# Kernel optimization log

Hardware: AMD Instinct MI355X
Metric: run time of the kernel (lower is better)

## Reference

```python
import jax, jax.numpy as jnp
import numpy as np

N_OR = 8          # orientations of the SE(2) discretization
BN_EPS = 1e-5


def _rotate_kernel(W, theta):
    """Rotate a spatial kernel [..., k, k] about its center by theta.
    Bilinear interpolation, zeros outside the kernel support."""
    k = W.shape[-1]
    c = (k - 1) / 2.0
    ys, xs = jnp.meshgrid(jnp.arange(k, dtype=jnp.float32) - c,
                          jnp.arange(k, dtype=jnp.float32) - c, indexing="ij")
    cos, sin = jnp.cos(theta), jnp.sin(theta)
    sy = cos * ys - sin * xs + c   # source coords: rotate sample grid by -theta
    sx = sin * ys + cos * xs + c
    y0 = jnp.floor(sy).astype(jnp.int32)
    x0 = jnp.floor(sx).astype(jnp.int32)
    wy = (sy - y0).astype(W.dtype)
    wx = (sx - x0).astype(W.dtype)

    def gather(yi, xi):
        valid = ((yi >= 0) & (yi < k) & (xi >= 0) & (xi < k)).astype(W.dtype)
        yc = jnp.clip(yi, 0, k - 1)
        xc = jnp.clip(xi, 0, k - 1)
        return W[..., yc, xc] * valid

    return (gather(y0, x0) * (1 - wy) * (1 - wx)
            + gather(y0, x0 + 1) * (1 - wy) * wx
            + gather(y0 + 1, x0) * wy * (1 - wx)
            + gather(y0 + 1, x0 + 1) * wy * wx)


def _thetas():
    return 2.0 * jnp.pi * jnp.arange(N_OR, dtype=jnp.float32) / N_OR


def _lift(x, W):
    """LiftM2Cartesian. x: [B,Cin,H,W] (pre-padded), W: [Cout,Cin,k,k].
    Returns [B,Cout,8,H',W']."""
    Wr = jax.vmap(lambda t: _rotate_kernel(W, t))(_thetas())  # [8,Cout,Cin,k,k]
    co = W.shape[0]
    Wf = Wr.reshape((N_OR * co,) + W.shape[1:])
    y = jax.lax.conv_general_dilated(x, Wf, (1, 1), "VALID",
                                     dimension_numbers=("NCHW", "OIHW", "NCHW"))
    B, _, H, Wd = y.shape
    return y.reshape(B, N_OR, co, H, Wd).transpose(0, 2, 1, 3, 4)


def _gconv(x, K):
    """ConvM2Cartesian. x: [B,Cin,8,H,W] (spatially pre-padded),
    K: [Cout,Cin,8,k,k]. Output orientation m uses the kernel spatially
    rotated by theta_m with the orientation axis cyclically shifted by m."""
    cout, cin, _, k, _ = K.shape
    # orient_idx[m, o] = (o - m) mod 8
    orient_idx = (jnp.arange(N_OR)[None, :] - jnp.arange(N_OR)[:, None]) % N_OR
    Kshift = jnp.moveaxis(K[:, :, orient_idx], 2, 0)        # [8m,Cout,Cin,8o,k,k]
    Km = jax.vmap(_rotate_kernel)(Kshift, _thetas())         # [8m,Cout,Cin,8o,k,k]
    Kf = Km.reshape(N_OR * cout, cin * N_OR, k, k)
    B, _, _, H, Wd = x.shape
    xf = x.reshape(B, cin * N_OR, H, Wd)
    y = jax.lax.conv_general_dilated(xf, Kf, (1, 1), "VALID",
                                     dimension_numbers=("NCHW", "OIHW", "NCHW"))
    Ho, Wo = y.shape[-2:]
    return y.reshape(B, N_OR, cout, Ho, Wo).transpose(0, 2, 1, 3, 4)


def _bn3d(x, gamma, beta):
    """BatchNorm3d (training-mode batch statistics). x: [B,C,O,H,W]."""
    mean = jnp.mean(x, axis=(0, 2, 3, 4), keepdims=True)
    var = jnp.mean((x - mean) ** 2, axis=(0, 2, 3, 4), keepdims=True)
    g = gamma.reshape(1, -1, 1, 1, 1)
    b = beta.reshape(1, -1, 1, 1, 1)
    return g * (x - mean) * jax.lax.rsqrt(var + BN_EPS) + b


def _pad_m2(x, p):
    return jnp.pad(x, ((0, 0), (0, 0), (0, 0), (p, p), (p, p)), mode="reflect")


def setup_inputs() -> dict:
    key = jax.random.key(0)
    ks = jax.random.split(key, 8)
    c = 16
    cin = 3
    x = jax.random.normal(ks[0], (2, cin, 256, 256), dtype=jnp.float32)
    lift_w = jax.random.normal(ks[1], (c, cin, 7, 7), dtype=jnp.float32) / np.sqrt(cin * 49)
    w1 = jax.random.normal(ks[2], (c, c, N_OR, 5, 5), dtype=jnp.float32) / np.sqrt(c * N_OR * 25)
    w2 = jax.random.normal(ks[3], (c, c, N_OR, 5, 5), dtype=jnp.float32) / np.sqrt(c * N_OR * 25)
    w3 = jax.random.normal(ks[4], (c, c, N_OR, 5, 5), dtype=jnp.float32) / np.sqrt(c * N_OR * 25)
    w4 = jax.random.normal(ks[5], (c, c, N_OR, 1, 1), dtype=jnp.float32) / np.sqrt(c * N_OR)
    final_w = jax.random.normal(ks[6], (1, c), dtype=jnp.float32) / np.sqrt(c)
    ones = jnp.ones((c,), dtype=jnp.float32)
    zeros = jnp.zeros((c,), dtype=jnp.float32)
    return {"x": x, "lift_w": lift_w, "w1": w1, "w2": w2, "w3": w3, "w4": w4,
            "final_w": final_w,
            "g0": ones, "b0": zeros, "g1": ones, "b1": zeros, "g2": ones,
            "b2": zeros, "g3": ones, "b3": zeros, "g4": ones, "b4": zeros}


def reference(x, lift_w, w1, w2, w3, w4, final_w,
              g0, b0, g1, b1, g2, b2, g3, b3, g4, b4):
    # lift: ReflectionPad2d(3) -> LiftM2Cartesian(7) -> BN3d -> ReLU
    xp = jnp.pad(x, ((0, 0), (0, 0), (3, 3), (3, 3)), mode="reflect")
    h = jax.nn.relu(_bn3d(_lift(xp, lift_w), g0, b0))          # [B,16,8,H,W]
    # conv1..3: ReflectionPadM2(2) -> ConvM2Cartesian(5) -> BN3d -> ReLU (Dropout3d is identity in eval)
    h = jax.nn.relu(_bn3d(_gconv(_pad_m2(h, 2), w1), g1, b1))
    h = jax.nn.relu(_bn3d(_gconv(_pad_m2(h, 2), w2), g2, b2))
    h = jax.nn.relu(_bn3d(_gconv(_pad_m2(h, 2), w3), g3, b3))
    # conv4: 1x1 group conv -> BN3d -> ReLU
    h = jax.nn.relu(_bn3d(_gconv(h, w4), g4, b4))
    # MaxProjectM2: max over orientation axis
    h = jnp.max(h, axis=2)                                     # [B,16,H,W]
    # final 1x1 conv (no bias) + sigmoid
    return jax.nn.sigmoid(jnp.einsum("bchw,oc->bohw", h, final_w))
```

## Files before the change

kernel.cpp:

```cpp
#include <hip/hip_runtime.h>
#include <hip/hip_bf16.h>
#include <math.h>

#define HW 65536
#define WID 256
#define NOR 8
#define PLANE_C (NOR * HW)
#define PLANE_B (16 * NOR * HW)
#define BN_N 1048576.0f
#define NHWC_STRIDE 136

typedef __attribute__((ext_vector_type(8)))  short  short8;
typedef __attribute__((ext_vector_type(4)))  short  short4v;
typedef __attribute__((ext_vector_type(16))) float  float16;
typedef __attribute__((ext_vector_type(4)))  float  float4v;

__device__ __forceinline__ float b2f(short s) {
    union { unsigned int u; float f; } c;
    c.u = ((unsigned int)(unsigned short)s) << 16;
    return c.f;
}
__device__ __forceinline__ short f2b(float f) {
    union { __hip_bfloat16 h; short s; } c;
    c.h = __float2bfloat16(f);
    return c.s;
}

__global__ void detect_k(const void* __restrict__ x, int* __restrict__ flag) {
    __shared__ int bad;
    if (threadIdx.x == 0) bad = 0;
    __syncthreads();
    const __hip_bfloat16* p = (const __hip_bfloat16*)x;
    for (int i = threadIdx.x; i < 4096; i += 256) {
        float v = __bfloat162float(p[i]);
        if (!(fabsf(v) < 1e4f)) atomicOr(&bad, 1);
    }
    __syncthreads();
    if (threadIdx.x == 0) *flag = bad ? 0 : 1;
}

#define CVT_TOTAL 551392
__global__ void cvt_all_k(const void* p0, const void* p1, const void* p2, const void* p3,
                          const void* p4, const void* p5, const void* p6, const void* p7,
                          const void* p8, const void* p9, const void* p10, const void* p11,
                          const void* p12, const void* p13, const void* p14, const void* p15,
                          const void* p16, float* __restrict__ dst, const int* __restrict__ flag) {
    int i = blockIdx.x * 512 + threadIdx.x;
    if (i >= CVT_TOTAL) return;
    const void* src; int off;
    if      (i < 393216) { src = p0;  off = 0; }
    else if (i < 395568) { src = p1;  off = 393216; }
    else if (i < 446768) { src = p2;  off = 395568; }
    else if (i < 497968) { src = p3;  off = 446768; }
    else if (i < 549168) { src = p4;  off = 497968; }
    else if (i < 551216) { src = p5;  off = 549168; }
    else if (i < 551232) { src = p6;  off = 551216; }
    else if (i < 551248) { src = p7;  off = 551232; }
    else if (i < 551264) { src = p8;  off = 551248; }
    else if (i < 551280) { src = p9;  off = 551264; }
    else if (i < 551296) { src = p10; off = 551280; }
    else if (i < 551312) { src = p11; off = 551296; }
    else if (i < 551328) { src = p12; off = 551312; }
    else if (i < 551344) { src = p13; off = 551328; }
    else if (i < 551360) { src = p14; off = 551344; }
    else if (i < 551376) { src = p15; off = 551360; }
    else                 { src = p16; off = 551376; }
    int j = i - off;
    dst[i] = (*flag) ? __bfloat162float(((const __hip_bfloat16*)src)[j])
                     : ((const float*)src)[j];
}

__device__ float rot_sample(const float* __restrict__ W, int k, float theta, int i, int j) {
    float c = 0.5f * (float)(k - 1);
    float ys = (float)i - c, xs = (float)j - c;
    float cs = cosf(theta), sn = sinf(theta);
    float sy = cs * ys - sn * xs + c;
    float sx = sn * ys + cs * xs + c;
    float fy = floorf(sy), fx = floorf(sx);
    int y0 = (int)fy, x0 = (int)fx;
    float wy = sy - fy, wx = sx - fx;
    float v00 = (y0 >= 0 && y0 < k && x0 >= 0 && x0 < k)                 ? W[y0 * k + x0]           : 0.f;
    float v01 = (y0 >= 0 && y0 < k && x0 + 1 >= 0 && x0 + 1 < k)         ? W[y0 * k + x0 + 1]       : 0.f;
    float v10 = (y0 + 1 >= 0 && y0 + 1 < k && x0 >= 0 && x0 < k)         ? W[(y0 + 1) * k + x0]     : 0.f;
    float v11 = (y0 + 1 >= 0 && y0 + 1 < k && x0 + 1 >= 0 && x0 + 1 < k) ? W[(y0 + 1) * k + x0 + 1] : 0.f;
    return v00 * (1 - wy) * (1 - wx) + v01 * (1 - wy) * wx
         + v10 * wy * (1 - wx) + v11 * wy * wx;
}

__device__ __forceinline__ float theta_of(int m) {
    return (6.2831855f * (float)m) / 8.0f;
}

__device__ __forceinline__ int mirror(int i) {
    i = i < 0 ? -i : i;
    return i >= WID ? (2 * WID - 2 - i) : i;
}

#define PK_BLIFT 20480
#define PK_BG 409600
#define PK_TOTAL (PK_BLIFT + 3 * PK_BG + 16384)
__global__ void mega_pack_k(const float* __restrict__ lwF, const float* __restrict__ w1F,
                            const float* __restrict__ w2F, const float* __restrict__ w3F,
                            const float* __restrict__ w4F,
                            __hip_bfloat16* __restrict__ Blift, __hip_bfloat16* __restrict__ Bg1,
                            __hip_bfloat16* __restrict__ Bg2, __hip_bfloat16* __restrict__ Bg3,
                            __hip_bfloat16* __restrict__ B1, float* __restrict__ statsL) {
    int idx = blockIdx.x * 256 + threadIdx.x;
    if (idx < 160) statsL[idx] = 0.f;
    if (idx >= PK_TOTAL) return;
    if (idx < PK_BLIFT) {
        int n = idx / 160, k = idx % 160;
        float v = 0.f;
        if (k < 147) {
            int c = n >> 3, o = n & 7;
            int ci = k / 49, s = k % 49;
            v = rot_sample(lwF + (c * 3 + ci) * 49, 7, theta_of(o), s / 7, s % 7);
        }
        Blift[idx] = __float2bfloat16(v);
        return;
    }
    idx -= PK_BLIFT;
    if (idx < 3 * PK_BG) {
        int l = idx / PK_BG;
        int r = idx - l * PK_BG;
        const float* w = (l == 0) ? w1F : ((l == 1) ? w2F : w3F);
        __hip_bfloat16* Bg = (l == 0) ? Bg1 : ((l == 1) ? Bg2 : Bg3);
        int j = r & 7;
        int n = (r >> 3) & 127;
        int kc4 = (r >> 10) & 3;
        int sq = r >> 12;
        int s = sq % 25, q = sq / 25;
        int ch = q * 32 + kc4 * 8 + j;
        int co = n >> 3, m = n & 7, ci = ch >> 3, o = ch & 7;
        int oo = (o - m + 8) & 7;
        Bg[r] = __float2bfloat16(
            rot_sample(w + ((co * 16 + ci) * 8 + oo) * 25, 5, theta_of(m), s / 5, s % 5));
        return;
    }
    idx -= 3 * PK_BG;
    {
        int n = idx >> 7, ch = idx & 127;
        int co = n >> 3, m = n & 7, ci = ch >> 3, o = ch & 7;
        B1[idx] = __float2bfloat16(w4F[(co * 16 + ci) * 8 + ((o - m + 8) & 7)]);
    }
}

__device__ __forceinline__ void stats_reduce8(const float16* acc, int lane, int l31,
                                              float* sred) {
#pragma unroll
    for (int nt = 0; nt < 4; nt++) {
        float sv = 0.f, s2v = 0.f;
#pragma unroll
        for (int g = 0; g < 2; g++)
#pragma unroll
            for (int r = 0; r < 16; r++) {
                float v = acc[g * 4 + nt][r];
                sv += v;
                s2v += v * v;
            }
#pragma unroll
        for (int off = 1; off <= 4; off <<= 1) {
            sv += __shfl_xor(sv, off);
            s2v += __shfl_xor(s2v, off);
        }
        sv += __shfl_xor(sv, 32);
        s2v += __shfl_xor(s2v, 32);
        if ((lane & 39) == 0) {
            int c = nt * 4 + (l31 >> 3);
            atomicAdd(&sred[c], sv);
            atomicAdd(&sred[16 + c], s2v);
        }
    }
}

__global__ __launch_bounds__(256, 2) void lift_fused_k(const float* __restrict__ xF,
                                                       const __hip_bfloat16* __restrict__ Bh,
                                                       __hip_bfloat16* __restrict__ nh_out,
                                                       float* __restrict__ stats) {
    __shared__ float Xs[3 * 484];
    __shared__ short tb[32768];
    __shared__ float sred[32];
    const short* B = (const short*)Bh;
    int tid = threadIdx.x;
    if (tid < 32) sred[tid] = 0.f;
    int tile = blockIdx.x;
    int b = blockIdx.y;
    int tx0 = (tile & 15) << 4, ty0 = (tile >> 4) << 4;
    for (int i = tid; i < 1452; i += 256) {
        int ci = i / 484, p = i - ci * 484;
        int yl = p / 22, xl = p - yl * 22;
        int gy = mirror(ty0 - 3 + yl), gx = mirror(tx0 - 3 + xl);
        Xs[i] = xF[((size_t)b * 3 + ci) * HW + gy * WID + gx];
    }
    __syncthreads();
    int wave = tid >> 6, lane = tid & 63;
    int l31 = lane & 31, half = lane >> 5;
    float16 acc[8];
#pragma unroll
    for (int i = 0; i < 8; i++) acc[i] = (float16)0.f;
    int pxl0 = wave * 64 + l31;
    int py0 = pxl0 >> 4, px0 = pxl0 & 15;
    int py1 = (pxl0 + 32) >> 4, px1 = (pxl0 + 32) & 15;
    const short* bp = B + (size_t)l31 * 160 + half * 8;
#pragma unroll
    for (int ks = 0; ks < 10; ks++) {
        short8 a0, a1;
#pragma unroll
        for (int j = 0; j < 8; j++) {
            int k = ks * 16 + half * 8 + j;
            float v0 = 0.f, v1 = 0.f;
            if (k < 147) {
                int ci = (k < 49) ? 0 : ((k < 98) ? 1 : 2);
                int s = k - ci * 49;
                int sy = s / 7, sx = s - sy * 7;
                v0 = Xs[ci * 484 + (py0 + sy) * 22 + px0 + sx];
                v1 = Xs[ci * 484 + (py1 + sy) * 22 + px1 + sx];
            }
            a0[j] = f2b(v0);
            a1[j] = f2b(v1);
        }
#pragma unroll
        for (int nt = 0; nt < 4; nt++) {
            short8 bb = *(const short8*)(bp + nt * 32 * 160 + ks * 16);
            acc[nt]     = __builtin_amdgcn_mfma_f32_32x32x16_bf16(a0, bb, acc[nt], 0, 0, 0);
            acc[4 + nt] = __builtin_amdgcn_mfma_f32_32x32x16_bf16(a1, bb, acc[4 + nt], 0, 0, 0);
        }
    }
#pragma unroll
    for (int g = 0; g < 2; g++)
#pragma unroll
        for (int nt = 0; nt < 4; nt++) {
            int ch = nt * 32 + l31;
#pragma unroll
            for (int r4 = 0; r4 < 4; r4++) {
                int pxb = wave * 64 + g * 32 + 8 * r4 + 4 * half;
#pragma unroll
                for (int i = 0; i < 4; i++)
                    tb[(pxb + i) * 128 + ch] = f2b(acc[g * 4 + nt][r4 * 4 + i]);
            }
        }
    __syncthreads();
    short* outp = (short*)nh_out + (size_t)b * HW * NHWC_STRIDE;
    for (int i = tid; i < 4096; i += 256) {
        int pxl = i >> 4, seg = i & 15;
        int y = ty0 + (pxl >> 4), x = tx0 + (pxl & 15);
        *(short8*)(outp + ((size_t)y * WID + x) * NHWC_STRIDE + seg * 8) =
            *(const short8*)&tb[pxl * 128 + seg * 8];
    }
    stats_reduce8(acc, lane, l31, sred);
    __syncthreads();
    if (tid < 16) {
        atomicAdd(&stats[tid * 2], sred[tid]);
        atomicAdd(&stats[tid * 2 + 1], sred[16 + tid]);
    }
}

__global__ __launch_bounds__(256, 3) void gconv_mfma_k(const __hip_bfloat16* __restrict__ nh_in,
                                                       const __hip_bfloat16* __restrict__ Bgh,
                                                       __hip_bfloat16* __restrict__ nh_out,
                                                       const float* __restrict__ statsPrev,
                                                       const float* __restrict__ gPrev,
                                                       const float* __restrict__ bPrev,
                                                       float* __restrict__ statsNew) {
    __shared__ short Au[16384];
    __shared__ float ssl[32];
    __shared__ float sred[32];
    const short* nhwc = (const short*)nh_in;
    const short* Bg = (const short*)Bgh;
    int bid = blockIdx.x;
    int xcd = bid & 7, q2 = bid >> 3;
    int nhalf = q2 & 1, qt = q2 >> 1;
    int b = xcd >> 2, band = xcd & 3;
    int tx0 = (qt & 15) << 4;
    int ty0 = (band << 6) + ((qt >> 4) << 4);
    int tid = threadIdx.x;
    if (tid < 32) sred[tid] = 0.f;
    if (tid < 16) {
        float mean = statsPrev[tid * 2] / BN_N;
        float var = statsPrev[tid * 2 + 1] / BN_N - mean * mean;
        float sc = gPrev[tid] * rsqrtf(var + 1e-5f);
        ssl[tid * 2] = sc;
        ssl[tid * 2 + 1] = bPrev[tid] - mean * sc;
    }
    int w = tid >> 6, lane = tid & 63;
    int l15 = lane & 15, l4 = lane >> 4;
    float4v acc[16];
#pragma unroll
    for (int i = 0; i < 16; i++) acc[i] = (float4v)0.f;
    const size_t bbase = (size_t)b * HW;
    const int nb = nhalf << 6;

    for (int q = 0; q < 4; q++) {
        __syncthreads();
        for (int i = tid; i < 1600; i += 256) {
            int kc = i / 400, p = i - kc * 400;
            int yl = p / 20, xl = p - yl * 20;
            int gy = mirror(ty0 - 2 + yl);
            int gx = mirror(tx0 - 2 + xl);
            short8 raw = *(const short8*)(nhwc + (bbase + gy * WID + gx) * NHWC_STRIDE
                                          + q * 32 + kc * 8);
            int c = q * 4 + kc;
            float sc = ssl[c * 2], sh = ssl[c * 2 + 1];
            short8 ov;
#pragma unroll
            for (int e = 0; e < 8; e++)
                ov[e] = f2b(fmaxf(fmaf(b2f(raw[e]), sc, sh), 0.f));
            *(short8*)&Au[(kc * 441 + yl * 21 + xl) * 8] = ov;
        }
        __syncthreads();
        for (int s = 0; s < 25; s++) {
            int dy = s / 5 - 2, dx = s % 5 - 2;
            int abase = l4 * 441 + ((w << 2) + 2 + dy) * 21 + (l15 + 2 + dx);
            const short* brow = Bg + ((size_t)(((q * 25 + s) << 2) + l4) * 128 + nb + l15) * 8;
            short8 a0 = *(const short8*)&Au[abase * 8];
            short8 a1 = *(const short8*)&Au[(abase + 21) * 8];
            short8 a2 = *(const short8*)&Au[(abase + 42) * 8];
            short8 a3 = *(const short8*)&Au[(abase + 63) * 8];
#pragma unroll
            for (int nt = 0; nt < 4; nt++) {
                short8 bb = *(const short8*)(brow + nt * 128);
                acc[nt]      = __builtin_amdgcn_mfma_f32_16x16x32_bf16(a0, bb, acc[nt], 0, 0, 0);
                acc[4 + nt]  = __builtin_amdgcn_mfma_f32_16x16x32_bf16(a1, bb, acc[4 + nt], 0, 0, 0);
                acc[8 + nt]  = __builtin_amdgcn_mfma_f32_16x16x32_bf16(a2, bb, acc[8 + nt], 0, 0, 0);
                acc[12 + nt] = __builtin_amdgcn_mfma_f32_16x16x32_bf16(a3, bb, acc[12 + nt], 0, 0, 0);
            }
        }
    }

    __syncthreads();
#pragma unroll
    for (int ag = 0; ag < 4; ag++) {
        int pxb = ((w << 2) + ag) * 16 + (l4 << 2);
#pragma unroll
        for (int nt = 0; nt < 4; nt++) {
            int nl = nt * 16 + l15;
#pragma unroll
            for (int r = 0; r < 4; r++)
                Au[(pxb + r) * 64 + nl] = f2b(acc[ag * 4 + nt][r]);
        }
    }
    __syncthreads();
    short* outp = (short*)nh_out;
    for (int i = tid; i < 2048; i += 256) {
        int pxl = i >> 3, seg = i & 7;
        int y = ty0 + (pxl >> 4), x = tx0 + (pxl & 15);
        *(short8*)(outp + (bbase + y * WID + x) * NHWC_STRIDE + nb + seg * 8) =
            *(const short8*)&Au[pxl * 64 + seg * 8];
    }
#pragma unroll
    for (int nt = 0; nt < 4; nt++) {
        float sv = 0.f, s2v = 0.f;
#pragma unroll
        for (int ag = 0; ag < 4; ag++)
#pragma unroll
            for (int r = 0; r < 4; r++) {
                float v = acc[ag * 4 + nt][r];
                sv += v;
                s2v += v * v;
            }
#pragma unroll
        for (int off = 1; off <= 4; off <<= 1) {
            sv += __shfl_xor(sv, off);
            s2v += __shfl_xor(s2v, off);
        }
        sv += __shfl_xor(sv, 16);
        s2v += __shfl_xor(s2v, 16);
        sv += __shfl_xor(sv, 32);
        s2v += __shfl_xor(s2v, 32);
        if ((lane & 7) == 0 && l4 == 0) {
            int c = (nhalf << 3) + (nt << 1) + (l15 >> 3);
            atomicAdd(&sred[c], sv);
            atomicAdd(&sred[16 + c], s2v);
        }
    }
    __syncthreads();
    if (tid < 16) {
        atomicAdd(&statsNew[tid * 2], sred[tid]);
        atomicAdd(&statsNew[tid * 2 + 1], sred[16 + tid]);
    }
}

__global__ __launch_bounds__(256, 2) void conv1x1_gemm_k(const __hip_bfloat16* __restrict__ nh,
                                                         const __hip_bfloat16* __restrict__ B1h,
                                                         __hip_bfloat16* __restrict__ outP,
                                                         const float* __restrict__ statsPrev,
                                                         const float* __restrict__ gPrev,
                                                         const float* __restrict__ bPrev,
                                                         float* __restrict__ statsNew) {
    __shared__ float sred[32];
    __shared__ float ssl[32];
    const short* nhwc = (const short*)nh;
    const short* B1 = (const short*)B1h;
    int tid = threadIdx.x;
    if (tid < 32) sred[tid] = 0.f;
    if (tid < 16) {
        float mean = statsPrev[tid * 2] / BN_N;
        float var = statsPrev[tid * 2 + 1] / BN_N - mean * mean;
        float sc = gPrev[tid] * rsqrtf(var + 1e-5f);
        ssl[tid * 2] = sc;
        ssl[tid * 2 + 1] = bPrev[tid] - mean * sc;
    }
    __syncthreads();
    int b = blockIdx.y;
    int wave = tid >> 6, lane = tid & 63;
    int l31 = lane & 31, half = lane >> 5;
    int p0 = blockIdx.x * 256 + wave * 64;
    float16 acc[8];
#pragma unroll
    for (int i = 0; i < 8; i++) acc[i] = (float16)0.f;
    const short* a0p = nhwc + ((size_t)b * HW + p0 + l31) * NHWC_STRIDE + half * 8;
    const short* a1p = a0p + 32 * NHWC_STRIDE;
    const short* bp  = B1 + (size_t)l31 * 128 + half * 8;
#pragma unroll
    for (int ks = 0; ks < 8; ks++) {
        short8 r0 = *(const short8*)(a0p + ks * 16);
        short8 r1 = *(const short8*)(a1p + ks * 16);
        int c = ks * 2 + half;
        float sc = ssl[c * 2], sh = ssl[c * 2 + 1];
        short8 a0, a1;
#pragma unroll
        for (int e = 0; e < 8; e++) {
            a0[e] = f2b(fmaxf(fmaf(b2f(r0[e]), sc, sh), 0.f));
            a1[e] = f2b(fmaxf(fmaf(b2f(r1[e]), sc, sh), 0.f));
        }
#pragma unroll
        for (int nt = 0; nt < 4; nt++) {
            short8 bb = *(const short8*)(bp + nt * 32 * 128 + ks * 16);
            acc[nt]     = __builtin_amdgcn_mfma_f32_32x32x16_bf16(a0, bb, acc[nt], 0, 0, 0);
            acc[4 + nt] = __builtin_amdgcn_mfma_f32_32x32x16_bf16(a1, bb, acc[4 + nt], 0, 0, 0);
        }
    }
    short* outb = (short*)outP + (size_t)b * PLANE_B;
#pragma unroll
    for (int g = 0; g < 2; g++)
#pragma unroll
        for (int nt = 0; nt < 4; nt++) {
            int n = nt * 32 + l31;
#pragma unroll
            for (int r4 = 0; r4 < 4; r4++) {
                int base = 8 * r4 + 4 * half;
                short4v v;
                v[0] = f2b(acc[g * 4 + nt][r4 * 4 + 0]);
                v[1] = f2b(acc[g * 4 + nt][r4 * 4 + 1]);
                v[2] = f2b(acc[g * 4 + nt][r4 * 4 + 2]);
                v[3] = f2b(acc[g * 4 + nt][r4 * 4 + 3]);
                *(short4v*)(outb + (size_t)n * HW + p0 + g * 32 + base) = v;
            }
        }
    stats_reduce8(acc, lane, l31, sred);
    __syncthreads();
    if (tid < 16) {
        atomicAdd(&statsNew[tid * 2], sred[tid]);
        atomicAdd(&statsNew[tid * 2 + 1], sred[16 + tid]);
    }
}

__global__ void final_k(const __hip_bfloat16* __restrict__ inP, const float* __restrict__ stats,
                        const float* __restrict__ g, const float* __restrict__ beta,
                        const float* __restrict__ fw, void* __restrict__ out,
                        const int* __restrict__ flag) {
    __shared__ float ssl[32];
    if (threadIdx.x < 16) {
        int c = threadIdx.x;
        float mean = stats[c * 2] / BN_N;
        float var = stats[c * 2 + 1] / BN_N - mean * mean;
        float sc = g[c] * rsqrtf(var + 1e-5f);
        ssl[c * 2] = sc;
        ssl[c * 2 + 1] = beta[c] - mean * sc;
    }
    __syncthreads();
    int i = blockIdx.x * blockDim.x + threadIdx.x;
    int b = i >> 16, pix = i & 65535;
    const short* inp = (const short*)inP;
    float acc = 0.f;
#pragma unroll
    for (int co = 0; co < 16; co++) {
        float sc = ssl[co * 2], sh = ssl[co * 2 + 1];
        float mx = 0.f;
        const short* p = inp + (size_t)b * PLANE_B + (size_t)co * PLANE_C + pix;
#pragma unroll
        for (int m = 0; m < 8; m++) mx = fmaxf(mx, fmaf(b2f(p[m * HW]), sc, sh));
        acc = fmaf(fw[co], mx, acc);
    }
    float r = 1.f / (1.f + expf(-acc));
    if (*flag)
        ((__hip_bfloat16*)out)[i] = __float2bfloat16(r);
    else
        ((float*)out)[i] = r;
}

extern "C" void kernel_launch(void* const* d_in, const int* in_sizes, int n_in,
                              void* d_out, int out_size, void* d_ws, size_t ws_size,
                              hipStream_t stream) {
    float* ws = (float*)d_ws;
    __hip_bfloat16* planarB = (__hip_bfloat16*)ws;
    __hip_bfloat16* nhwcA = (__hip_bfloat16*)(ws + 8388608);
    __hip_bfloat16* nhwcB = (__hip_bfloat16*)(ws + 17301504);
    __hip_bfloat16* Bg1   = (__hip_bfloat16*)(ws + 26214400);
    __hip_bfloat16* Bg2   = (__hip_bfloat16*)(ws + 26419200);
    __hip_bfloat16* Bg3   = (__hip_bfloat16*)(ws + 26624000);
    __hip_bfloat16* Blift = (__hip_bfloat16*)(ws + 26828800);
    __hip_bfloat16* B1    = (__hip_bfloat16*)(ws + 26839040);
    float* xF  = ws + 26847232;
    float* lwF = xF + 393216;
    float* w1F = lwF + 2352;
    float* w2F = w1F + 51200;
    float* w3F = w2F + 51200;
    float* w4F = w3F + 51200;
    float* fwF = w4F + 2048;
    float* gbF = fwF + 16;
    float* statsL = ws + 27398624;
    int*   flag   = (int*)(statsL + 160);

    detect_k<<<1, 256, 0, stream>>>(d_in[0], flag);
    cvt_all_k<<<(CVT_TOTAL + 511) / 512, 512, 0, stream>>>(
        d_in[0], d_in[1], d_in[2], d_in[3], d_in[4], d_in[5], d_in[6], d_in[7], d_in[8],
        d_in[9], d_in[10], d_in[11], d_in[12], d_in[13], d_in[14], d_in[15], d_in[16],
        xF, flag);

    mega_pack_k<<<(PK_TOTAL + 255) / 256, 256, 0, stream>>>(
        lwF, w1F, w2F, w3F, w4F, Blift, Bg1, Bg2, Bg3, B1, statsL);

    lift_fused_k<<<dim3(256, 2), 256, 0, stream>>>(xF, Blift, nhwcA, statsL);

    __hip_bfloat16* Bgs[3] = {Bg1, Bg2, Bg3};
    __hip_bfloat16* nio[4] = {nhwcA, nhwcB, nhwcA, nhwcB};
    for (int l = 0; l < 3; l++) {
        gconv_mfma_k<<<1024, 256, 0, stream>>>(nio[l], Bgs[l], nio[l + 1],
                                               statsL + 32 * l, gbF + 32 * l, gbF + 32 * l + 16,
                                               statsL + 32 * (l + 1));
    }

    conv1x1_gemm_k<<<dim3(256, 2), 256, 0, stream>>>(nio[3], B1, planarB,
                                                     statsL + 96, gbF + 96, gbF + 112,
                                                     statsL + 128);

    final_k<<<(2 * HW) / 256, 256, 0, stream>>>(planarB, statsL + 128, gbF + 128, gbF + 144,
                                                fwF, d_out, flag);
}
```

Before: 502.8 us.

## Compute both output-channel halves per gconv block to halve input tile loads

Each gconv block now produces all 128 output channels for its 16x16 pixel tile instead of one half. The halo input load, BN-apply and ReLU conversion are therefore done once per tile rather than twice, and the grid shrinks from 1024 to 512 blocks. Each wave holds 32 accumulators and reuses 8 A fragments across 4 B tiles. The cost is doubled LDS, more registers and occupancy bounds lowered from 3 to 2, with fewer blocks to spread across CUs.

```diff
diff --git a/kernel.cpp b/kernel.cpp
--- a/kernel.cpp
+++ b/kernel.cpp
@@ -255,21 +255,20 @@
     }
 }
 
-__global__ __launch_bounds__(256, 3) void gconv_mfma_k(const __hip_bfloat16* __restrict__ nh_in,
+__global__ __launch_bounds__(256, 2) void gconv_mfma_k(const __hip_bfloat16* __restrict__ nh_in,
                                                        const __hip_bfloat16* __restrict__ Bgh,
                                                        __hip_bfloat16* __restrict__ nh_out,
                                                        const float* __restrict__ statsPrev,
                                                        const float* __restrict__ gPrev,
                                                        const float* __restrict__ bPrev,
                                                        float* __restrict__ statsNew) {
-    __shared__ short Au[16384];
+    __shared__ short Au[32768];
     __shared__ float ssl[32];
     __shared__ float sred[32];
     const short* nhwc = (const short*)nh_in;
     const short* Bg = (const short*)Bgh;
     int bid = blockIdx.x;
-    int xcd = bid & 7, q2 = bid >> 3;
-    int nhalf = q2 & 1, qt = q2 >> 1;
+    int xcd = bid & 7, qt = bid >> 3;
     int b = xcd >> 2, band = xcd & 3;
     int tx0 = (qt & 15) << 4;
     int ty0 = (band << 6) + ((qt >> 4) << 4);
@@ -283,23 +282,24 @@
         ssl[tid * 2 + 1] = bPrev[tid] - mean * sc;
     }
     int w = tid >> 6, lane = tid & 63;
+    int pxg = w & 1, nhf = w >> 1;
     int l15 = lane & 15, l4 = lane >> 4;
-    float4v acc[16];
-#pragma unroll
-    for (int i = 0; i < 16; i++) acc[i] = (float4v)0.f;
+    float4v acc[32];
+#pragma unroll
+    for (int i = 0; i < 32; i++) acc[i] = (float4v)0.f;
     const size_t bbase = (size_t)b * HW;
-    const int nb = nhalf << 6;
-
-    for (int q = 0; q < 4; q++) {
+    const int nb = nhf << 6;
+
+    for (int h = 0; h < 2; h++) {
         __syncthreads();
-        for (int i = tid; i < 1600; i += 256) {
+        for (int i = tid; i < 3200; i += 256) {
             int kc = i / 400, p = i - kc * 400;
             int yl = p / 20, xl = p - yl * 20;
             int gy = mirror(ty0 - 2 + yl);
             int gx = mirror(tx0 - 2 + xl);
             short8 raw = *(const short8*)(nhwc + (bbase + gy * WID + gx) * NHWC_STRIDE
-                                          + q * 32 + kc * 8);
-            int c = q * 4 + kc;
+                                          + h * 64 + kc * 8);
+            int c = h * 8 + kc;
             float sc = ssl[c * 2], sh = ssl[c * 2 + 1];
             short8 ov;
 #pragma unroll
@@ -310,51 +310,55 @@
         __syncthreads();
         for (int s = 0; s < 25; s++) {
             int dy = s / 5 - 2, dx = s % 5 - 2;
-            int abase = l4 * 441 + ((w << 2) + 2 + dy) * 21 + (l15 + 2 + dx);
-            const short* brow = Bg + ((size_t)(((q * 25 + s) << 2) + l4) * 128 + nb + l15) * 8;
-            short8 a0 = *(const short8*)&Au[abase * 8];
-            short8 a1 = *(const short8*)&Au[(abase + 21) * 8];
-            short8 a2 = *(const short8*)&Au[(abase + 42) * 8];
-            short8 a3 = *(const short8*)&Au[(abase + 63) * 8];
-#pragma unroll
-            for (int nt = 0; nt < 4; nt++) {
-                short8 bb = *(const short8*)(brow + nt * 128);
-                acc[nt]      = __builtin_amdgcn_mfma_f32_16x16x32_bf16(a0, bb, acc[nt], 0, 0, 0);
-                acc[4 + nt]  = __builtin_amdgcn_mfma_f32_16x16x32_bf16(a1, bb, acc[4 + nt], 0, 0, 0);
-                acc[8 + nt]  = __builtin_amdgcn_mfma_f32_16x16x32_bf16(a2, bb, acc[8 + nt], 0, 0, 0);
-                acc[12 + nt] = __builtin_amdgcn_mfma_f32_16x16x32_bf16(a3, bb, acc[12 + nt], 0, 0, 0);
+#pragma unroll
+            for (int kq = 0; kq < 2; kq++) {
+                int abase = (kq * 4 + l4) * 441 + ((pxg << 3) + 2 + dy) * 21 + (l15 + 2 + dx);
+                const short* brow = Bg
+                    + ((size_t)(((((h * 2 + kq) * 25 + s) << 2) + l4)) * 128 + nb + l15) * 8;
+                short8 a[8];
+#pragma unroll
+                for (int r = 0; r < 8; r++)
+                    a[r] = *(const short8*)&Au[(abase + r * 21) * 8];
+#pragma unroll
+                for (int nt = 0; nt < 4; nt++) {
+                    short8 bb = *(const short8*)(brow + nt * 128);
+#pragma unroll
+                    for (int r = 0; r < 8; r++)
+                        acc[r * 4 + nt] = __builtin_amdgcn_mfma_f32_16x16x32_bf16(
+                            a[r], bb, acc[r * 4 + nt], 0, 0, 0);
+                }
             }
         }
     }
 
     __syncthreads();
 #pragma unroll
-    for (int ag = 0; ag < 4; ag++) {
-        int pxb = ((w << 2) + ag) * 16 + (l4 << 2);
+    for (int r = 0; r < 8; r++) {
+        int pxl = ((pxg << 3) + r) * 16 + (l4 << 2);
 #pragma unroll
         for (int nt = 0; nt < 4; nt++) {
-            int nl = nt * 16 + l15;
-#pragma unroll
-            for (int r = 0; r < 4; r++)
-                Au[(pxb + r) * 64 + nl] = f2b(acc[ag * 4 + nt][r]);
+            int n = nb + nt * 16 + l15;
+#pragma unroll
+            for (int e = 0; e < 4; e++)
+                Au[(pxl + e) * 128 + n] = f2b(acc[r * 4 + nt][e]);
         }
     }
     __syncthreads();
     short* outp = (short*)nh_out;
-    for (int i = tid; i < 2048; i += 256) {
-        int pxl = i >> 3, seg = i & 7;
+    for (int i = tid; i < 4096; i += 256) {
+        int pxl = i >> 4, seg = i & 15;
         int y = ty0 + (pxl >> 4), x = tx0 + (pxl & 15);
-        *(short8*)(outp + (bbase + y * WID + x) * NHWC_STRIDE + nb + seg * 8) =
-            *(const short8*)&Au[pxl * 64 + seg * 8];
+        *(short8*)(outp + (bbase + y * WID + x) * NHWC_STRIDE + seg * 8) =
+            *(const short8*)&Au[pxl * 128 + seg * 8];
     }
 #pragma unroll
     for (int nt = 0; nt < 4; nt++) {
         float sv = 0.f, s2v = 0.f;
 #pragma unroll
-        for (int ag = 0; ag < 4; ag++)
-#pragma unroll
-            for (int r = 0; r < 4; r++) {
-                float v = acc[ag * 4 + nt][r];
+        for (int r = 0; r < 8; r++)
+#pragma unroll
+            for (int e = 0; e < 4; e++) {
+                float v = acc[r * 4 + nt][e];
                 sv += v;
                 s2v += v * v;
             }
@@ -368,7 +372,7 @@
         sv += __shfl_xor(sv, 32);
         s2v += __shfl_xor(s2v, 32);
         if ((lane & 7) == 0 && l4 == 0) {
-            int c = (nhalf << 3) + (nt << 1) + (l15 >> 3);
+            int c = (nhf << 3) + (nt << 1) + (l15 >> 3);
             atomicAdd(&sred[c], sv);
             atomicAdd(&sred[16 + c], s2v);
         }
@@ -526,9 +530,9 @@
     __hip_bfloat16* Bgs[3] = {Bg1, Bg2, Bg3};
     __hip_bfloat16* nio[4] = {nhwcA, nhwcB, nhwcA, nhwcB};
     for (int l = 0; l < 3; l++) {
-        gconv_mfma_k<<<1024, 256, 0, stream>>>(nio[l], Bgs[l], nio[l + 1],
-                                               statsL + 32 * l, gbF + 32 * l, gbF + 32 * l + 16,
-                                               statsL + 32 * (l + 1));
+        gconv_mfma_k<<<512, 256, 0, stream>>>(nio[l], Bgs[l], nio[l + 1],
+                                              statsL + 32 * l, gbF + 32 * l, gbF + 32 * l + 16,
+                                              statsL + 32 * (l + 1));
     }
 
     conv1x1_gemm_k<<<dim3(256, 2), 256, 0, stream>>>(nio[3], B1, planarB,
```

New measurement: 458.1 us. -8.9%, faster.
